# Optimization experiments

Measured on AMD Instinct MI355X. Metric: run time of the kernel, lower is better.

Reference implementation:

```python
import jax, jax.numpy as jnp
import numpy as np

N, E = 50000, 800000
DIN, DH, DOUT = 128, 128, 64


def setup_inputs() -> dict:
    key = jax.random.key(0)
    k = jax.random.split(key, 6)
    node_features = jax.random.normal(k[0], (N, DIN), dtype=jnp.float32)
    edge_src = jax.random.randint(k[1], (E,), 0, N)
    edge_dst = jax.random.randint(k[2], (E,), 0, N)
    # Glorot-ish init for the two GCNConv weight matrices, zero bias (PyG default bias=True)
    W1 = jax.random.normal(k[3], (DIN, DH), dtype=jnp.float32) * (1.0 / np.sqrt(DIN))
    b1 = jnp.zeros((DH,), dtype=jnp.float32)
    W2 = jax.random.normal(k[4], (DH, DOUT), dtype=jnp.float32) * (1.0 / np.sqrt(DH))
    b2 = jnp.zeros((DOUT,), dtype=jnp.float32)
    return {"node_features": node_features, "edge_src": edge_src, "edge_dst": edge_dst,
            "W1": W1, "b1": b1, "W2": W2, "b2": b2}


def gcn_conv(x, W, b, src, dst, n):
    """PyG GCNConv: add self-loops, symmetric D^-1/2 (A+I) D^-1/2 normalization."""
    xw = x @ W  # [n, d_out]
    loops = jnp.arange(n, dtype=src.dtype)
    s = jnp.concatenate([src, loops])  # edges + self-loops
    d = jnp.concatenate([dst, loops])
    deg = jax.ops.segment_sum(jnp.ones_like(d, dtype=xw.dtype), d, num_segments=n)
    dinv = jnp.where(deg > 0, jax.lax.rsqrt(deg), 0.0)
    norm = dinv[s] * dinv[d]  # [E + n]
    msg = xw[s] * norm[:, None]  # gather + scale (memory-bound)
    out = jax.ops.segment_sum(msg, d, num_segments=n)  # scatter-add
    return out + b


def reference(node_features, edge_src, edge_dst, W1, b1, W2, b2):
    n = node_features.shape[0]
    h = gcn_conv(node_features, W1, b1, edge_src, edge_dst, n)
    h = jax.nn.relu(h)  # dropout omitted (inference / eval mode)
    h = gcn_conv(h, W2, b2, edge_src, edge_dst, n)
    # EdgePredictor: per-edge dot product of endpoint representations
    score = jnp.sum(h[edge_src] * h[edge_dst], axis=-1)  # [E]
    return score
```

## Files before the change

### kernel.cpp

```cpp
#include <hip/hip_runtime.h>
#include <hip/hip_bf16.h>
#include <type_traits>


#define DIN 128
#define DH  128
#define DOUT 64
#define CAP 8192

typedef __attribute__((ext_vector_type(8))) short short8;
typedef __attribute__((ext_vector_type(4))) float floatx4;

__device__ inline float2 bf2_to_f2(unsigned u) {
    union { unsigned i; float f; } a, b;
    a.i = u << 16;
    b.i = u & 0xffff0000u;
    return make_float2(a.f, b.f);
}
__device__ inline float bf_to_f(unsigned short u) {
    union { unsigned i; float f; } a;
    a.i = ((unsigned)u) << 16;
    return a.f;
}
__device__ inline unsigned short f_to_bf(float f) {
    union { float f; unsigned i; } v; v.f = f;
    unsigned r = v.i + 0x7fffu + ((v.i >> 16) & 1u);
    return (unsigned short)(r >> 16);
}

__global__ __launch_bounds__(256) void place_kernel(const int* __restrict__ src,
                                                    const int* __restrict__ dst,
                                                    int* __restrict__ cursor,
                                                    uint2* __restrict__ tmp, int E) {
    __shared__ int hist[256];
    __shared__ int cur[256];
    int t = threadIdx.x;
    hist[t] = 0;
    __syncthreads();
    int base = blockIdx.x * 4096 + t;
    int d[16];
#pragma unroll
    for (int it = 0; it < 16; ++it) {
        int e = base + it * 256;
        d[it] = (e < E) ? dst[e] : -1;
        if (d[it] >= 0) atomicAdd(&hist[d[it] >> 8], 1);
    }
    __syncthreads();
    if (hist[t]) cur[t] = atomicAdd(&cursor[t], hist[t]);
    __syncthreads();
#pragma unroll
    for (int it = 0; it < 16; ++it) {
        int e = base + it * 256;
        if (d[it] >= 0) {
            int bkt = d[it] >> 8;
            int r = atomicAdd(&cur[bkt], 1);
            if (r < CAP)
                tmp[(size_t)bkt * CAP + r] =
                    make_uint2((unsigned)src[e] | ((unsigned)(d[it] & 255) << 16),
                               (unsigned)e);
        }
    }
}

__global__ __launch_bounds__(256) void bucket_csr_kernel(const uint2* __restrict__ tmp,
                                                         const int* __restrict__ cursor,
                                                         int* __restrict__ row_beg,
                                                         int* __restrict__ row_end,
                                                         float* __restrict__ dinv,
                                                         int* __restrict__ col,
                                                         int* __restrict__ eidx, int N) {
    __shared__ int hist[256], cur[256], pfx[256];
    __shared__ unsigned ebuf[CAP];
    __shared__ unsigned ibuf[CAP];
    __shared__ unsigned ssrc[CAP];
    __shared__ unsigned sidx[CAP];
    int b = blockIdx.x, t = threadIdx.x;
    int size = cursor[b];
    if (size > CAP) size = CAP;
    size_t rbase = (size_t)b * CAP;
    hist[t] = 0;
    __syncthreads();
    for (int i = t; i < size; i += 256) {
        uint2 e = tmp[rbase + i];
        ebuf[i] = e.x;
        ibuf[i] = e.y;
        atomicAdd(&hist[e.x >> 16], 1);
    }
    __syncthreads();
    int v = hist[t];
    pfx[t] = v;
    __syncthreads();
    for (int off = 1; off < 256; off <<= 1) {
        int u = (t >= off) ? pfx[t - off] : 0;
        __syncthreads();
        pfx[t] += u;
        __syncthreads();
    }
    int ex = pfx[t] - v;
    cur[t] = ex;
    int node = b * 256 + t;
    if (node < N) {
        row_beg[node] = (int)rbase + ex;
        row_end[node] = (int)rbase + ex + v;
        dinv[node] = rsqrtf((float)(v + 1));
    }
    __syncthreads();
    for (int i = t; i < size; i += 256) {
        int r = atomicAdd(&cur[ebuf[i] >> 16], 1);
        ssrc[r] = ebuf[i] & 0xffffu;
        sidx[r] = ibuf[i];
    }
    __syncthreads();
    for (int i = t; i < size; i += 256) {
        col[rbase + i]  = (int)ssrc[i];
        eidx[rbase + i] = (int)sidx[i];
    }
}

template <int COLS, typename XT>
__global__ __launch_bounds__(256) void mfma_gemm_kernel(const XT* __restrict__ X,
                                                        const float* __restrict__ W,
                                                        const float* __restrict__ dinv,
                                                        unsigned short* __restrict__ Y,
                                                        int nrows) {
    constexpr int KP = 136;
    __shared__ unsigned short Xs[128 * KP];
    __shared__ unsigned short Wt[COLS * KP];
    int tid = threadIdx.x;
    int row0 = blockIdx.x * 128;

    if constexpr (std::is_same_v<XT, float>) {
#pragma unroll
        for (int it = 0; it < 16; ++it) {
            int idx = it * 256 + tid;
            int r = idx >> 5;
            int c4 = (idx & 31) * 4;
            int gr = row0 + r; if (gr >= nrows) gr = nrows - 1;
            float4 v = *(const float4*)(X + (size_t)gr * 128 + c4);
            ushort4 p;
            p.x = f_to_bf(v.x); p.y = f_to_bf(v.y);
            p.z = f_to_bf(v.z); p.w = f_to_bf(v.w);
            *(ushort4*)&Xs[r * KP + c4] = p;
        }
    } else {
#pragma unroll
        for (int it = 0; it < 8; ++it) {
            int idx = it * 256 + tid;
            int r = idx >> 4;
            int c8 = (idx & 15) * 8;
            int gr = row0 + r; if (gr >= nrows) gr = nrows - 1;
            uint4 v = *(const uint4*)(X + (size_t)gr * 128 + c8);
            *(uint4*)&Xs[r * KP + c8] = v;
        }
    }
#pragma unroll
    for (int it = 0; it < COLS / 8; ++it) {
        int idx = it * 256 + tid;
        int n = idx >> 5;
        int k4 = (idx & 31) * 4;
        ushort4 p;
        p.x = f_to_bf(W[(size_t)(k4 + 0) * COLS + n]);
        p.y = f_to_bf(W[(size_t)(k4 + 1) * COLS + n]);
        p.z = f_to_bf(W[(size_t)(k4 + 2) * COLS + n]);
        p.w = f_to_bf(W[(size_t)(k4 + 3) * COLS + n]);
        *(ushort4*)&Wt[n * KP + k4] = p;
    }
    __syncthreads();

    constexpr int CT = COLS / 16;
    int wv = tid >> 6, lane = tid & 63;
    int lr = lane & 15;
    int lk = (lane >> 4) * 8;
    int rw = wv * 32;

    floatx4 acc[2][CT];
#pragma unroll
    for (int rt = 0; rt < 2; ++rt)
#pragma unroll
        for (int ct = 0; ct < CT; ++ct) acc[rt][ct] = (floatx4){0.f, 0.f, 0.f, 0.f};

#pragma unroll
    for (int kk = 0; kk < 128; kk += 32) {
        short8 a[2], b[CT];
#pragma unroll
        for (int rt = 0; rt < 2; ++rt)
            a[rt] = *(const short8*)&Xs[(rw + rt * 16 + lr) * KP + kk + lk];
#pragma unroll
        for (int ct = 0; ct < CT; ++ct)
            b[ct] = *(const short8*)&Wt[(ct * 16 + lr) * KP + kk + lk];
#pragma unroll
        for (int rt = 0; rt < 2; ++rt)
#pragma unroll
            for (int ct = 0; ct < CT; ++ct)
                acc[rt][ct] = __builtin_amdgcn_mfma_f32_16x16x32_bf16(
                    a[rt], b[ct], acc[rt][ct], 0, 0, 0);
    }

#pragma unroll
    for (int rt = 0; rt < 2; ++rt) {
#pragma unroll
        for (int i = 0; i < 4; ++i) {
            int grow = row0 + rw + rt * 16 + (lane >> 4) * 4 + i;
            if (grow >= nrows) continue;
            float dv = dinv[grow];
#pragma unroll
            for (int ct = 0; ct < CT; ++ct)
                Y[(size_t)grow * COLS + ct * 16 + lr] =
                    f_to_bf(acc[rt][ct][i] * dv);
        }
    }
}

template <int D, bool RELU>
__global__ __launch_bounds__(256) void agg_kernel(const unsigned short* __restrict__ y,
                                                  const int* __restrict__ row_beg,
                                                  const int* __restrict__ row_end,
                                                  const int* __restrict__ col,
                                                  const float* __restrict__ dinv,
                                                  const float* __restrict__ bias,
                                                  unsigned short* __restrict__ out, int n) {
    constexpr int V = D / 64;
    int w = (blockIdx.x * 256 + threadIdx.x) >> 6;
    int lane = threadIdx.x & 63;
    if (w >= n) return;
    float acc[V];
    if constexpr (V == 2) {
        float2 t = bf2_to_f2(*(const unsigned*)(y + (size_t)w * D + lane * 2));
        acc[0] = t.x; acc[1] = t.y;
    } else {
        acc[0] = bf_to_f(y[(size_t)w * D + lane]);
    }
    int beg = row_beg[w], end = row_end[w];
    int i = beg;
    for (; i + 8 <= end; i += 8) {
        int s[8];
#pragma unroll
        for (int u = 0; u < 8; ++u) s[u] = col[i + u];
        if constexpr (V == 2) {
            unsigned tv[8];
#pragma unroll
            for (int u = 0; u < 8; ++u)
                tv[u] = *(const unsigned*)(y + (size_t)s[u] * D + lane * 2);
#pragma unroll
            for (int u = 0; u < 8; ++u) {
                float2 f = bf2_to_f2(tv[u]);
                acc[0] += f.x; acc[1] += f.y;
            }
        } else {
            unsigned short tv[8];
#pragma unroll
            for (int u = 0; u < 8; ++u) tv[u] = y[(size_t)s[u] * D + lane];
#pragma unroll
            for (int u = 0; u < 8; ++u) acc[0] += bf_to_f(tv[u]);
        }
    }
    for (; i < end; ++i) {
        int s = col[i];
        if constexpr (V == 2) {
            float2 f = bf2_to_f2(*(const unsigned*)(y + (size_t)s * D + lane * 2));
            acc[0] += f.x; acc[1] += f.y;
        } else {
            acc[0] += bf_to_f(y[(size_t)s * D + lane]);
        }
    }
    float dv = dinv[w];
    if constexpr (V == 2) {
        float r0 = fmaf(dv, acc[0], bias[lane * 2]);
        float r1 = fmaf(dv, acc[1], bias[lane * 2 + 1]);
        if (RELU) { r0 = fmaxf(r0, 0.f); r1 = fmaxf(r1, 0.f); }
        unsigned pk = (unsigned)f_to_bf(r0) | ((unsigned)f_to_bf(r1) << 16);
        *(unsigned*)(out + (size_t)w * D + lane * 2) = pk;
    } else {
        float r = fmaf(dv, acc[0], bias[lane]);
        if (RELU) r = fmaxf(r, 0.f);
        out[(size_t)w * D + lane] = f_to_bf(r);
    }
}

__global__ __launch_bounds__(256) void score_csr_kernel(const unsigned short* __restrict__ h2,
                                                        const int* __restrict__ row_beg,
                                                        const int* __restrict__ row_end,
                                                        const int* __restrict__ col,
                                                        const int* __restrict__ eidx,
                                                        float* __restrict__ out, int n) {
    int w = (blockIdx.x * 256 + threadIdx.x) >> 6;
    int lane = threadIdx.x & 63;
    if (w >= n) return;
    int q = lane & 7;
    uint4 hd = *(const uint4*)(h2 + (size_t)w * 64 + q * 8);
    float d0[8];
    { float2 f;
      f = bf2_to_f2(hd.x); d0[0] = f.x; d0[1] = f.y;
      f = bf2_to_f2(hd.y); d0[2] = f.x; d0[3] = f.y;
      f = bf2_to_f2(hd.z); d0[4] = f.x; d0[5] = f.y;
      f = bf2_to_f2(hd.w); d0[6] = f.x; d0[7] = f.y; }
    int beg = row_beg[w], end = row_end[w];
    int g = lane >> 3;
    for (int i = beg; i < end; i += 8) {
        int ei = i + g;
        bool ok = ei < end;
        int s = ok ? col[ei] : 0;
        uint4 hs = *(const uint4*)(h2 + (size_t)s * 64 + q * 8);
        float v = 0.f;
        float2 f;
        f = bf2_to_f2(hs.x); v = fmaf(d0[0], f.x, v); v = fmaf(d0[1], f.y, v);
        f = bf2_to_f2(hs.y); v = fmaf(d0[2], f.x, v); v = fmaf(d0[3], f.y, v);
        f = bf2_to_f2(hs.z); v = fmaf(d0[4], f.x, v); v = fmaf(d0[5], f.y, v);
        f = bf2_to_f2(hs.w); v = fmaf(d0[6], f.x, v); v = fmaf(d0[7], f.y, v);
        v += __shfl_xor(v, 4);
        v += __shfl_xor(v, 2);
        v += __shfl_xor(v, 1);
        if (ok && q == 0) out[eidx[ei]] = v;
    }
}

extern "C" void kernel_launch(void* const* d_in, const int* in_sizes, int n_in,
                              void* d_out, int out_size, void* d_ws, size_t ws_size,
                              hipStream_t stream) {
    const float* X   = (const float*)d_in[0];
    const int*   src = (const int*)d_in[1];
    const int*   dst = (const int*)d_in[2];
    const float* W1  = (const float*)d_in[3];
    const float* b1  = (const float*)d_in[4];
    const float* W2  = (const float*)d_in[5];
    const float* b2  = (const float*)d_in[6];
    float* score = (float*)d_out;

    const int N = in_sizes[0] / DIN;
    const int E = in_sizes[1];
    const int nbuck = (N + 255) / 256;
    const int EB = (E + 4095) / 4096;

    auto align = [](size_t x) { return (x + 255) & ~(size_t)255; };
    char* p = (char*)d_ws;
    int*   cursor  = (int*)p;               p += align(256 * 4);
    int*   row_beg = (int*)p;               p += align((size_t)N * 4);
    int*   row_end = (int*)p;               p += align((size_t)N * 4);
    float* dinv    = (float*)p;             p += align((size_t)N * 4);
    int*   col     = (int*)p;               p += align((size_t)nbuck * CAP * 4);
    int*   eidx    = (int*)p;               p += align((size_t)nbuck * CAP * 4);
    uint2* tmp     = (uint2*)p;             p += align((size_t)nbuck * CAP * 8);
    unsigned short* y1 = (unsigned short*)p; p += align((size_t)N * DH * 2);
    unsigned short* h1 = (unsigned short*)p; p += align((size_t)N * DH * 2);
    unsigned short* y2 = y1;
    unsigned short* h2 = y1 + (size_t)N * DOUT;

    hipMemsetAsync(cursor, 0, 256 * 4, stream);

    place_kernel<<<EB, 256, 0, stream>>>(src, dst, cursor, tmp, E);
    bucket_csr_kernel<<<nbuck, 256, 0, stream>>>(tmp, cursor, row_beg, row_end,
                                                 dinv, col, eidx, N);

    int gemm_blocks = (N + 127) / 128;
    mfma_gemm_kernel<DH, float><<<gemm_blocks, 256, 0, stream>>>(X, W1, dinv, y1, N);

    int agg_blocks = (N + 3) / 4;
    agg_kernel<DH, true><<<agg_blocks, 256, 0, stream>>>(y1, row_beg, row_end,
                                                         col, dinv, b1, h1, N);

    mfma_gemm_kernel<DOUT, unsigned short><<<gemm_blocks, 256, 0, stream>>>(h1, W2, dinv, y2, N);
    agg_kernel<DOUT, false><<<agg_blocks, 256, 0, stream>>>(y2, row_beg, row_end,
                                                            col, dinv, b2, h2, N);

    score_csr_kernel<<<agg_blocks, 256, 0, stream>>>(h2, row_beg, row_end,
                                                     col, eidx, score, N);
}
```

Measured before the change: 246.5 us.

## Split layer-1 features into two 64-wide halves and aggregate each separately

The first GEMM now writes its 128-wide output as two separate 64-column arrays, and layer-1 aggregation runs as two passes, one per half. Each half-row is 128 bytes, so the gathered working set per pass is halved and is more likely to stay cache-resident. The new half kernel splits a wavefront into four groups of 16 lanes, each group handling a different edge with 8-byte loads, and combines the groups with shuffles. The CSR build also scatters col/eidx straight to global memory, dropping the shared-memory staging and one barrier at the cost of uncoalesced writes. The trade is an extra kernel launch and a second read of the CSR arrays.

```diff
diff --git a/kernel.cpp b/kernel.cpp
--- a/kernel.cpp
+++ b/kernel.cpp
@@ -72,8 +72,6 @@
     __shared__ int hist[256], cur[256], pfx[256];
     __shared__ unsigned ebuf[CAP];
     __shared__ unsigned ibuf[CAP];
-    __shared__ unsigned ssrc[CAP];
-    __shared__ unsigned sidx[CAP];
     int b = blockIdx.x, t = threadIdx.x;
     int size = cursor[b];
     if (size > CAP) size = CAP;
@@ -107,13 +105,8 @@
     __syncthreads();
     for (int i = t; i < size; i += 256) {
         int r = atomicAdd(&cur[ebuf[i] >> 16], 1);
-        ssrc[r] = ebuf[i] & 0xffffu;
-        sidx[r] = ibuf[i];
-    }
-    __syncthreads();
-    for (int i = t; i < size; i += 256) {
-        col[rbase + i]  = (int)ssrc[i];
-        eidx[rbase + i] = (int)sidx[i];
+        col[rbase + r]  = (int)(ebuf[i] & 0xffffu);
+        eidx[rbase + r] = (int)ibuf[i];
     }
 }
 
@@ -121,7 +114,8 @@
 __global__ __launch_bounds__(256) void mfma_gemm_kernel(const XT* __restrict__ X,
                                                         const float* __restrict__ W,
                                                         const float* __restrict__ dinv,
-                                                        unsigned short* __restrict__ Y,
+                                                        unsigned short* __restrict__ Ya,
+                                                        unsigned short* __restrict__ Yb,
                                                         int nrows) {
     constexpr int KP = 136;
     __shared__ unsigned short Xs[128 * KP];
@@ -204,77 +198,94 @@
             if (grow >= nrows) continue;
             float dv = dinv[grow];
 #pragma unroll
-            for (int ct = 0; ct < CT; ++ct)
-                Y[(size_t)grow * COLS + ct * 16 + lr] =
-                    f_to_bf(acc[rt][ct][i] * dv);
-        }
-    }
-}
-
-template <int D, bool RELU>
-__global__ __launch_bounds__(256) void agg_kernel(const unsigned short* __restrict__ y,
-                                                  const int* __restrict__ row_beg,
-                                                  const int* __restrict__ row_end,
-                                                  const int* __restrict__ col,
-                                                  const float* __restrict__ dinv,
-                                                  const float* __restrict__ bias,
-                                                  unsigned short* __restrict__ out, int n) {
-    constexpr int V = D / 64;
+            for (int ct = 0; ct < CT; ++ct) {
+                unsigned short val = f_to_bf(acc[rt][ct][i] * dv);
+                if constexpr (COLS == 128) {
+                    unsigned short* Yp = (ct < 4) ? Ya : Yb;
+                    Yp[(size_t)grow * 64 + (ct & 3) * 16 + lr] = val;
+                } else {
+                    Ya[(size_t)grow * 64 + ct * 16 + lr] = val;
+                }
+            }
+        }
+    }
+}
+
+__global__ __launch_bounds__(256) void agg1_half_kernel(const unsigned short* __restrict__ y,
+                                                        const int* __restrict__ row_beg,
+                                                        const int* __restrict__ row_end,
+                                                        const int* __restrict__ col,
+                                                        const float* __restrict__ dinv,
+                                                        const float* __restrict__ bias,
+                                                        unsigned short* __restrict__ out,
+                                                        int n) {
     int w = (blockIdx.x * 256 + threadIdx.x) >> 6;
     int lane = threadIdx.x & 63;
     if (w >= n) return;
-    float acc[V];
-    if constexpr (V == 2) {
-        float2 t = bf2_to_f2(*(const unsigned*)(y + (size_t)w * D + lane * 2));
-        acc[0] = t.x; acc[1] = t.y;
-    } else {
-        acc[0] = bf_to_f(y[(size_t)w * D + lane]);
-    }
+    int q = lane & 15;
+    int g = lane >> 4;
+    float a0 = 0.f, a1 = 0.f, a2 = 0.f, a3 = 0.f;
+    int beg = row_beg[w], end = row_end[w];
+    for (int i = beg; i < end; i += 8) {
+        int e0 = i + g, e1 = i + 4 + g;
+        if (e0 < end) {
+            int s = col[e0];
+            uint2 u = *(const uint2*)(y + (size_t)s * 64 + q * 4);
+            float2 f0 = bf2_to_f2(u.x), f1 = bf2_to_f2(u.y);
+            a0 += f0.x; a1 += f0.y; a2 += f1.x; a3 += f1.y;
+        }
+        if (e1 < end) {
+            int s = col[e1];
+            uint2 u = *(const uint2*)(y + (size_t)s * 64 + q * 4);
+            float2 f0 = bf2_to_f2(u.x), f1 = bf2_to_f2(u.y);
+            a0 += f0.x; a1 += f0.y; a2 += f1.x; a3 += f1.y;
+        }
+    }
+    a0 += __shfl_xor(a0, 16); a0 += __shfl_xor(a0, 32);
+    a1 += __shfl_xor(a1, 16); a1 += __shfl_xor(a1, 32);
+    a2 += __shfl_xor(a2, 16); a2 += __shfl_xor(a2, 32);
+    a3 += __shfl_xor(a3, 16); a3 += __shfl_xor(a3, 32);
+    if (g == 0) {
+        uint2 us = *(const uint2*)(y + (size_t)w * 64 + q * 4);
+        float2 s0 = bf2_to_f2(us.x), s1 = bf2_to_f2(us.y);
+        float dv = dinv[w];
+        float r0 = fmaxf(fmaf(dv, a0 + s0.x, bias[q * 4 + 0]), 0.f);
+        float r1 = fmaxf(fmaf(dv, a1 + s0.y, bias[q * 4 + 1]), 0.f);
+        float r2 = fmaxf(fmaf(dv, a2 + s1.x, bias[q * 4 + 2]), 0.f);
+        float r3 = fmaxf(fmaf(dv, a3 + s1.y, bias[q * 4 + 3]), 0.f);
+        uint2 pk;
+        pk.x = (unsigned)f_to_bf(r0) | ((unsigned)f_to_bf(r1) << 16);
+        pk.y = (unsigned)f_to_bf(r2) | ((unsigned)f_to_bf(r3) << 16);
+        *(uint2*)(out + (size_t)w * 128 + q * 4) = pk;
+    }
+}
+
+__global__ __launch_bounds__(256) void agg2_kernel(const unsigned short* __restrict__ y,
+                                                   const int* __restrict__ row_beg,
+                                                   const int* __restrict__ row_end,
+                                                   const int* __restrict__ col,
+                                                   const float* __restrict__ dinv,
+                                                   const float* __restrict__ bias,
+                                                   unsigned short* __restrict__ out, int n) {
+    int w = (blockIdx.x * 256 + threadIdx.x) >> 6;
+    int lane = threadIdx.x & 63;
+    if (w >= n) return;
+    float acc = bf_to_f(y[(size_t)w * 64 + lane]);
     int beg = row_beg[w], end = row_end[w];
     int i = beg;
     for (; i + 8 <= end; i += 8) {
         int s[8];
 #pragma unroll
         for (int u = 0; u < 8; ++u) s[u] = col[i + u];
-        if constexpr (V == 2) {
-            unsigned tv[8];
-#pragma unroll
-            for (int u = 0; u < 8; ++u)
-                tv[u] = *(const unsigned*)(y + (size_t)s[u] * D + lane * 2);
-#pragma unroll
-            for (int u = 0; u < 8; ++u) {
-                float2 f = bf2_to_f2(tv[u]);
-                acc[0] += f.x; acc[1] += f.y;
-            }
-        } else {
-            unsigned short tv[8];
-#pragma unroll
-            for (int u = 0; u < 8; ++u) tv[u] = y[(size_t)s[u] * D + lane];
-#pragma unroll
-            for (int u = 0; u < 8; ++u) acc[0] += bf_to_f(tv[u]);
-        }
-    }
-    for (; i < end; ++i) {
-        int s = col[i];
-        if constexpr (V == 2) {
-            float2 f = bf2_to_f2(*(const unsigned*)(y + (size_t)s * D + lane * 2));
-            acc[0] += f.x; acc[1] += f.y;
-        } else {
-            acc[0] += bf_to_f(y[(size_t)s * D + lane]);
-        }
-    }
-    float dv = dinv[w];
-    if constexpr (V == 2) {
-        float r0 = fmaf(dv, acc[0], bias[lane * 2]);
-        float r1 = fmaf(dv, acc[1], bias[lane * 2 + 1]);
-        if (RELU) { r0 = fmaxf(r0, 0.f); r1 = fmaxf(r1, 0.f); }
-        unsigned pk = (unsigned)f_to_bf(r0) | ((unsigned)f_to_bf(r1) << 16);
-        *(unsigned*)(out + (size_t)w * D + lane * 2) = pk;
-    } else {
-        float r = fmaf(dv, acc[0], bias[lane]);
-        if (RELU) r = fmaxf(r, 0.f);
-        out[(size_t)w * D + lane] = f_to_bf(r);
-    }
+        unsigned short tv[8];
+#pragma unroll
+        for (int u = 0; u < 8; ++u) tv[u] = y[(size_t)s[u] * 64 + lane];
+#pragma unroll
+        for (int u = 0; u < 8; ++u) acc += bf_to_f(tv[u]);
+    }
+    for (; i < end; ++i) acc += bf_to_f(y[(size_t)col[i] * 64 + lane]);
+    float r = fmaf(dinv[w], acc, bias[lane]);
+    out[(size_t)w * 64 + lane] = f_to_bf(r);
 }
 
 __global__ __launch_bounds__(256) void score_csr_kernel(const unsigned short* __restrict__ h2,
@@ -340,10 +351,11 @@
     int*   col     = (int*)p;               p += align((size_t)nbuck * CAP * 4);
     int*   eidx    = (int*)p;               p += align((size_t)nbuck * CAP * 4);
     uint2* tmp     = (uint2*)p;             p += align((size_t)nbuck * CAP * 8);
-    unsigned short* y1 = (unsigned short*)p; p += align((size_t)N * DH * 2);
-    unsigned short* h1 = (unsigned short*)p; p += align((size_t)N * DH * 2);
-    unsigned short* y2 = y1;
-    unsigned short* h2 = y1 + (size_t)N * DOUT;
+    unsigned short* y1a = (unsigned short*)p; p += align((size_t)N * 64 * 2);
+    unsigned short* y1b = (unsigned short*)p; p += align((size_t)N * 64 * 2);
+    unsigned short* h1  = (unsigned short*)p; p += align((size_t)N * DH * 2);
+    unsigned short* y2  = y1a;
+    unsigned short* h2  = y1b;
 
     hipMemsetAsync(cursor, 0, 256 * 4, stream);
 
@@ -352,15 +364,20 @@
                                                  dinv, col, eidx, N);
 
     int gemm_blocks = (N + 127) / 128;
-    mfma_gemm_kernel<DH, float><<<gemm_blocks, 256, 0, stream>>>(X, W1, dinv, y1, N);
+    mfma_gemm_kernel<DH, float><<<gemm_blocks, 256, 0, stream>>>(X, W1, dinv,
+                                                                 y1a, y1b, N);
 
     int agg_blocks = (N + 3) / 4;
-    agg_kernel<DH, true><<<agg_blocks, 256, 0, stream>>>(y1, row_beg, row_end,
-                                                         col, dinv, b1, h1, N);
-
-    mfma_gemm_kernel<DOUT, unsigned short><<<gemm_blocks, 256, 0, stream>>>(h1, W2, dinv, y2, N);
-    agg_kernel<DOUT, false><<<agg_blocks, 256, 0, stream>>>(y2, row_beg, row_end,
-                                                            col, dinv, b2, h2, N);
+    agg1_half_kernel<<<agg_blocks, 256, 0, stream>>>(y1a, row_beg, row_end, col,
+                                                     dinv, b1, h1, N);
+    agg1_half_kernel<<<agg_blocks, 256, 0, stream>>>(y1b, row_beg, row_end, col,
+                                                     dinv, b1 + 64, h1 + 64, N);
+
+    mfma_gemm_kernel<DOUT, unsigned short><<<gemm_blocks, 256, 0, stream>>>(
+        h1, W2, dinv, y2, y2, N);
+
+    agg2_kernel<<<agg_blocks, 256, 0, stream>>>(y2, row_beg, row_end, col,
+                                                dinv, b2, h2, N);
 
     score_csr_kernel<<<agg_blocks, 256, 0, stream>>>(h2, row_beg, row_end,
                                                      col, eidx, score, N);
```

New measurement: 273.5 us. 11.0% more time.
